# Optimization experiments

Measured on AMD Instinct MI355X. Metric: run time of the kernel, lower is better.

Reference implementation:

```python
import jax, jax.numpy as jnp
import numpy as np


def setup_inputs() -> dict:
    key = jax.random.key(0)
    k1, k2, k3, k4, k5 = jax.random.split(key, 5)
    N, L, H = 512, 512, 768
    num_texts = 32
    hidden_states = jax.random.normal(k1, (N, L, H), dtype=jnp.float32)
    attention_mask = jax.random.randint(k2, (N, L), 0, 2).astype(jnp.int32)
    sample_map = jnp.sort(jax.random.randint(k3, (N,), 0, num_texts).astype(jnp.int64))
    Wq = jax.random.normal(k4, (H, H), dtype=jnp.float32) * (1.0 / np.sqrt(H))
    bq = jnp.zeros((H,), dtype=jnp.float32)
    Wk = jax.random.normal(k5, (H, H), dtype=jnp.float32) * (1.0 / np.sqrt(H))
    bk = jnp.zeros((H,), dtype=jnp.float32)
    return {
        'hidden_states': hidden_states,
        'attention_mask': attention_mask,
        'sample_map': sample_map,
        'Wq': Wq, 'bq': bq, 'Wk': Wk, 'bk': bk,
        'num_texts': num_texts,
    }


def _attn_pool(hidden_states, mask, Wq, bq, Wk, bk):
    # hidden_states: [N, L, H]; mask: [N, L]
    H = hidden_states.shape[-1]
    # Q from mean over sequence (unmasked mean, as in original)
    q = jnp.einsum('nh,oh->no', hidden_states.mean(axis=1), Wq) + bq   # [N, H]
    k = jnp.einsum('nlh,oh->nlo', hidden_states, Wk) + bk              # [N, L, H]
    scores = jnp.einsum('nh,nlh->nl', q, k) / jnp.sqrt(jnp.float32(H))  # [N, L]
    scores = jnp.where(mask == 0, jnp.float32(-1e9), scores)
    alphas = jax.nn.softmax(scores, axis=1)                            # [N, L]
    return jnp.einsum('nl,nlh->nh', alphas, hidden_states)             # [N, H]


def reference(hidden_states, attention_mask, sample_map, Wq, bq, Wk, bk, num_texts):
    # dropout is identity in eval mode
    pooled = _attn_pool(hidden_states, attention_mask, Wq, bq, Wk, bk)  # [N, H]
    seg = sample_map.astype(jnp.int32)
    sums = jax.ops.segment_sum(pooled, seg, num_segments=num_texts)     # [T, H]
    counts = jax.ops.segment_sum(jnp.ones((pooled.shape[0],), pooled.dtype), seg,
                                 num_segments=num_texts)                # [T]
    counts = jnp.clip(counts, 1.0, None)
    return sums / counts[:, None]
```

## Files before the change

### kernel.cpp

```cpp
#include <hip/hip_runtime.h>
#include <math.h>

#define HDIM 768
#define LMAX 512

__device__ __forceinline__ float dot4(const float4 a, const float4 b) {
  return a.x * b.x + a.y * b.y + a.z * b.z + a.w * b.w;
}
__device__ __forceinline__ void fma4(float4& a, const float s, const float4 b) {
  a.x += s * b.x; a.y += s * b.y; a.z += s * b.z; a.w += s * b.w;
}
__device__ __forceinline__ void scale4(float4& a, const float s) {
  a.x *= s; a.y *= s; a.z *= s; a.w *= s;
}

__global__ void zero_flags(unsigned* flags) {
  if (threadIdx.x < 4) flags[threadIdx.x] = 0u;
}

__global__ __launch_bounds__(256) void detect_flags(const unsigned* __restrict__ mask_w,
                                                    const unsigned* __restrict__ smap_w,
                                                    unsigned* __restrict__ flags,
                                                    int mask_words, int smap_words) {
  const int gtid = blockIdx.x * blockDim.x + threadIdx.x;
  const int gsz = gridDim.x * blockDim.x;
  unsigned acc = 0;
  for (int i = gtid; i < mask_words / 2; i += gsz) acc |= mask_w[2 * i + 1];
  if (acc) atomicOr(&flags[0], 1u);
  unsigned acc2 = 0;
  for (int i = gtid; i < smap_words / 2; i += gsz) acc2 |= smap_w[2 * i + 1];
  if (acc2) atomicOr(&flags[1], 1u);
}

__global__ __launch_bounds__(384) void mean_kernel(const float* __restrict__ hs,
                                                   float* __restrict__ meanb, int L) {
  __shared__ float4 red2[HDIM / 4];
  const int n = blockIdx.x;
  const int tid = threadIdx.x;
  const int half = tid / 192, t = tid % 192;
  const float4* row = reinterpret_cast<const float4*>(hs) + (size_t)n * L * (HDIM / 4);
  float ax = 0.f, ay = 0.f, az = 0.f, aw = 0.f;
  int l = half;
  for (; l + 16 <= L; l += 16) {
    float4 u[8];
#pragma unroll
    for (int i = 0; i < 8; ++i) u[i] = row[(size_t)(l + 2 * i) * (HDIM / 4) + t];
#pragma unroll
    for (int i = 0; i < 8; ++i) { ax += u[i].x; ay += u[i].y; az += u[i].z; aw += u[i].w; }
  }
  for (; l < L; l += 2) {
    float4 u = row[(size_t)l * (HDIM / 4) + t];
    ax += u.x; ay += u.y; az += u.z; aw += u.w;
  }
  if (half == 1) { float4 o; o.x = ax; o.y = ay; o.z = az; o.w = aw; red2[t] = o; }
  __syncthreads();
  if (half == 0) {
    const float inv = 1.0f / (float)L;
    const float4 r = red2[t];
    float4 o;
    o.x = (ax + r.x) * inv; o.y = (ay + r.y) * inv;
    o.z = (az + r.z) * inv; o.w = (aw + r.w) * inv;
    reinterpret_cast<float4*>(meanb + (size_t)n * HDIM)[t] = o;
  }
}

__global__ __launch_bounds__(256) void gemm_bt(const float* __restrict__ A,
                                               const float* __restrict__ B,
                                               const float* __restrict__ bias,
                                               float* __restrict__ C,
                                               int M, int Nn, int K) {
  __shared__ float As[32][17];
  __shared__ float Bs[64][17];
  const int m0 = blockIdx.x * 32, n0 = blockIdx.y * 64;
  const int idx = threadIdx.x;
  const int lc = idx & 15, lr = idx >> 4;
  const int tc = idx & 15, tr = idx >> 4;
  float c[2][4] = {{0.f,0.f,0.f,0.f},{0.f,0.f,0.f,0.f}};
  for (int k0 = 0; k0 < K; k0 += 16) {
    __syncthreads();
    As[lr][lc]      = A[(size_t)(m0 + lr) * K + k0 + lc];
    As[lr + 16][lc] = A[(size_t)(m0 + lr + 16) * K + k0 + lc];
    Bs[lr][lc]      = B[(size_t)(n0 + lr) * K + k0 + lc];
    Bs[lr + 16][lc] = B[(size_t)(n0 + lr + 16) * K + k0 + lc];
    Bs[lr + 32][lc] = B[(size_t)(n0 + lr + 32) * K + k0 + lc];
    Bs[lr + 48][lc] = B[(size_t)(n0 + lr + 48) * K + k0 + lc];
    __syncthreads();
#pragma unroll
    for (int k = 0; k < 16; ++k) {
      const float a0 = As[tr * 2][k], a1 = As[tr * 2 + 1][k];
      const float b0 = Bs[tc * 4][k], b1 = Bs[tc * 4 + 1][k];
      const float b2 = Bs[tc * 4 + 2][k], b3 = Bs[tc * 4 + 3][k];
      c[0][0] += a0 * b0; c[0][1] += a0 * b1; c[0][2] += a0 * b2; c[0][3] += a0 * b3;
      c[1][0] += a1 * b0; c[1][1] += a1 * b1; c[1][2] += a1 * b2; c[1][3] += a1 * b3;
    }
  }
#pragma unroll
  for (int j = 0; j < 4; ++j) {
    const float bv = bias ? bias[n0 + tc * 4 + j] : 0.f;
    C[(size_t)(m0 + tr * 2) * Nn + n0 + tc * 4 + j]     = c[0][j] + bv;
    C[(size_t)(m0 + tr * 2 + 1) * Nn + n0 + tc * 4 + j] = c[1][j] + bv;
  }
}

__global__ __launch_bounds__(256) void gemm_bn(const float* __restrict__ A,
                                               const float* __restrict__ B,
                                               float* __restrict__ C,
                                               int M, int Nn, int K) {
  __shared__ float As[32][17];
  __shared__ float Bs[16][65];
  const int m0 = blockIdx.x * 32, n0 = blockIdx.y * 64;
  const int idx = threadIdx.x;
  const int lc = idx & 15, lr = idx >> 4;
  const int bc = idx & 63, br = idx >> 6;
  const int tc = idx & 15, tr = idx >> 4;
  float c[2][4] = {{0.f,0.f,0.f,0.f},{0.f,0.f,0.f,0.f}};
  for (int k0 = 0; k0 < K; k0 += 16) {
    __syncthreads();
    As[lr][lc]      = A[(size_t)(m0 + lr) * K + k0 + lc];
    As[lr + 16][lc] = A[(size_t)(m0 + lr + 16) * K + k0 + lc];
    Bs[br][bc]      = B[(size_t)(k0 + br) * Nn + n0 + bc];
    Bs[br + 4][bc]  = B[(size_t)(k0 + br + 4) * Nn + n0 + bc];
    Bs[br + 8][bc]  = B[(size_t)(k0 + br + 8) * Nn + n0 + bc];
    Bs[br + 12][bc] = B[(size_t)(k0 + br + 12) * Nn + n0 + bc];
    __syncthreads();
#pragma unroll
    for (int k = 0; k < 16; ++k) {
      const float a0 = As[tr * 2][k], a1 = As[tr * 2 + 1][k];
      const float b0 = Bs[k][tc * 4], b1 = Bs[k][tc * 4 + 1];
      const float b2 = Bs[k][tc * 4 + 2], b3 = Bs[k][tc * 4 + 3];
      c[0][0] += a0 * b0; c[0][1] += a0 * b1; c[0][2] += a0 * b2; c[0][3] += a0 * b3;
      c[1][0] += a1 * b0; c[1][1] += a1 * b1; c[1][2] += a1 * b2; c[1][3] += a1 * b3;
    }
  }
#pragma unroll
  for (int j = 0; j < 4; ++j) {
    C[(size_t)(m0 + tr * 2) * Nn + n0 + tc * 4 + j]     = c[0][j];
    C[(size_t)(m0 + tr * 2 + 1) * Nn + n0 + tc * 4 + j] = c[1][j];
  }
}

__global__ __launch_bounds__(256) void attnpool(const float* __restrict__ hs,
                                                const unsigned* __restrict__ mask_w,
                                                const float* __restrict__ v,
                                                const unsigned* __restrict__ flags,
                                                float* __restrict__ pooled, int L) {
  __shared__ int   mrow[LMAX];
  __shared__ float red[4][HDIM];
  __shared__ float mw[4], sw[4];
  const int n = gridDim.x - 1 - blockIdx.x;
  const int tid = threadIdx.x;
  const int w = tid >> 6, lane = tid & 63;

  const int mask_is_i32 = (flags[0] != 0);
  for (int t = tid; t < L; t += 256) {
    const size_t idx = (size_t)n * L + t;
    mrow[t] = (int)(mask_is_i32 ? mask_w[idx] : mask_w[2 * idx]);
  }

  const float4* v4 = reinterpret_cast<const float4*>(v + (size_t)n * HDIM);
  const float4 vf0 = v4[lane], vf1 = v4[64 + lane], vf2 = v4[128 + lane];
  const float4* hs4 = reinterpret_cast<const float4*>(hs) + (size_t)n * L * (HDIM / 4);
  const float scale = 1.0f / sqrtf((float)HDIM);

  const int rpw = L / 4;
  const int r0 = w * rpw;
  float4 A0 = {0,0,0,0}, A1 = {0,0,0,0}, A2 = {0,0,0,0};
  float m = -3.0e38f, ssum = 0.f;
  float4 xa[4][3], xb[4][3];

  auto loadg = [&](float4 (&X)[4][3], int g) {
    const float4* rp = hs4 + (size_t)(r0 + g * 4) * (HDIM / 4);
#pragma unroll
    for (int q = 0; q < 4; ++q) {
      X[q][0] = rp[q * (HDIM / 4) + lane];
      X[q][1] = rp[q * (HDIM / 4) + 64 + lane];
      X[q][2] = rp[q * (HDIM / 4) + 128 + lane];
    }
  };
  auto procg = [&](float4 (&X)[4][3], int g) {
    float s[4];
#pragma unroll
    for (int q = 0; q < 4; ++q) {
      float p = dot4(X[q][0], vf0) + dot4(X[q][1], vf1) + dot4(X[q][2], vf2);
#pragma unroll
      for (int off = 32; off > 0; off >>= 1) p += __shfl_xor(p, off, 64);
      s[q] = (mrow[r0 + g * 4 + q] == 0) ? -1e9f : p * scale;
    }
    const float mc = fmaxf(fmaxf(s[0], s[1]), fmaxf(s[2], s[3]));
    if (mc > m) {
      const float f = __expf(m - mc);
      ssum *= f; scale4(A0, f); scale4(A1, f); scale4(A2, f);
      m = mc;
    }
#pragma unroll
    for (int q = 0; q < 4; ++q) {
      const float pq = __expf(s[q] - m);
      ssum += pq;
      fma4(A0, pq, X[q][0]); fma4(A1, pq, X[q][1]); fma4(A2, pq, X[q][2]);
    }
  };

  __syncthreads();
  loadg(xa, 0);
  const int ng = rpw / 4;
  for (int g = 0; g < ng; g += 2) {
    loadg(xb, g + 1);
    procg(xa, g);
    if (g + 2 < ng) loadg(xa, g + 2);
    procg(xb, g + 1);
  }

  if (lane == 0) { mw[w] = m; sw[w] = ssum; }
  {
    float* rw = red[w];
    *reinterpret_cast<float4*>(rw + 4 * lane)       = A0;
    *reinterpret_cast<float4*>(rw + 256 + 4 * lane) = A1;
    *reinterpret_cast<float4*>(rw + 512 + 4 * lane) = A2;
  }
  __syncthreads();
  const float M = fmaxf(fmaxf(mw[0], mw[1]), fmaxf(mw[2], mw[3]));
  const float f0 = __expf(mw[0] - M), f1 = __expf(mw[1] - M);
  const float f2 = __expf(mw[2] - M), f3 = __expf(mw[3] - M);
  const float S = sw[0] * f0 + sw[1] * f1 + sw[2] * f2 + sw[3] * f3;
  const float inv = 1.0f / S;
#pragma unroll
  for (int part = 0; part < 3; ++part) {
    const int col = part * 256 + tid;
    const float o = red[0][col] * f0 + red[1][col] * f1 + red[2][col] * f2 + red[3][col] * f3;
    pooled[(size_t)n * HDIM + col] = o * inv;
  }
}

__global__ __launch_bounds__(256) void segmean(const float* __restrict__ pooled,
                                               const void* __restrict__ smap,
                                               const unsigned* __restrict__ flags,
                                               float* __restrict__ out, int N) {
  const int t = blockIdx.x, tid = threadIdx.x;
  const int col = blockIdx.y * 256 + tid;
  const int smap_is_i32 = (flags[1] != 0);
  float a = 0.f;
  int cnt = 0;
  for (int i = 0; i < N; ++i) {
    const int s = smap_is_i32 ? ((const int*)smap)[i]
                              : (int)((const long long*)smap)[i];
    if (s == t) { a += pooled[(size_t)i * HDIM + col]; ++cnt; }
  }
  out[(size_t)t * HDIM + col] = a / (float)(cnt > 0 ? cnt : 1);
}

extern "C" void kernel_launch(void* const* d_in, const int* in_sizes, int n_in,
                              void* d_out, int out_size, void* d_ws, size_t ws_size,
                              hipStream_t stream) {
  const float*    hs     = (const float*)d_in[0];
  const unsigned* mask_w = (const unsigned*)d_in[1];
  const void*     smap   = d_in[2];
  const float*    Wq     = (const float*)d_in[3];
  const float*    bq     = (const float*)d_in[4];
  const float*    Wk     = (const float*)d_in[5];

  const int N = in_sizes[2];
  const int L = in_sizes[1] / N;
  const int H = in_sizes[4];
  const int T = out_size / H;

  float* meanb  = (float*)d_ws;
  float* q      = meanb + (size_t)N * H;
  float* v      = q     + (size_t)N * H;
  float* pooled = v     + (size_t)N * H;
  unsigned* flags = (unsigned*)(pooled + (size_t)N * H);
  (void)ws_size; (void)n_in;

  zero_flags<<<1, 64, 0, stream>>>(flags);
  detect_flags<<<64, 256, 0, stream>>>(mask_w, (const unsigned*)smap, flags,
                                       N * L, N);
  mean_kernel<<<N, 384, 0, stream>>>(hs, meanb, L);
  gemm_bt<<<dim3(N / 32, H / 64), 256, 0, stream>>>(meanb, Wq, bq, q, N, H, H);
  gemm_bn<<<dim3(N / 32, H / 64), 256, 0, stream>>>(q, Wk, v, N, H, H);
  attnpool<<<N, 256, 0, stream>>>(hs, mask_w, v, flags, pooled, L);
  segmean<<<dim3(T, 3), 256, 0, stream>>>(pooled, smap, flags, (float*)d_out, N);
}
```

Measured before the change: 439.1 us.

## Split attention pooling across two blocks per sample with async LDS staging

The attention-pooling kernel now launches two blocks per sample, each covering half the sequence. Rows are staged into double-buffered shared memory with global_load_lds async copies, four rows per chunk, and each wave computes one row's score. Partial max, sum and accumulator are written per half and combined in a merged segment-mean kernel. Flag detection writes per-block slots instead of atomics, which drops the zero-flags launch. The new path adds two barriers per four-row chunk and a per-chunk shared-memory round trip, which may throttle a memory-bound streaming loop.

After: 442.5 us. About the same (+0.8%).

```diff
diff --git a/kernel.cpp b/kernel.cpp
--- a/kernel.cpp
+++ b/kernel.cpp
@@ -2,34 +2,35 @@
 #include <math.h>
 
 #define HDIM 768
-#define LMAX 512
+#define CH 4
 
 __device__ __forceinline__ float dot4(const float4 a, const float4 b) {
   return a.x * b.x + a.y * b.y + a.z * b.z + a.w * b.w;
 }
-__device__ __forceinline__ void fma4(float4& a, const float s, const float4 b) {
-  a.x += s * b.x; a.y += s * b.y; a.z += s * b.z; a.w += s * b.w;
-}
-__device__ __forceinline__ void scale4(float4& a, const float s) {
-  a.x *= s; a.y *= s; a.z *= s; a.w *= s;
-}
-
-__global__ void zero_flags(unsigned* flags) {
-  if (threadIdx.x < 4) flags[threadIdx.x] = 0u;
-}
-
-__global__ __launch_bounds__(256) void detect_flags(const unsigned* __restrict__ mask_w,
+
+__device__ __forceinline__ void async16(const float* g, float* l) {
+  __builtin_amdgcn_global_load_lds(
+      (const __attribute__((address_space(1))) void*)g,
+      (__attribute__((address_space(3))) void*)l, 16, 0, 0);
+}
+
+__global__ __launch_bounds__(256) void detect_slots(const unsigned* __restrict__ mask_w,
                                                     const unsigned* __restrict__ smap_w,
-                                                    unsigned* __restrict__ flags,
+                                                    unsigned* __restrict__ slots,
                                                     int mask_words, int smap_words) {
-  const int gtid = blockIdx.x * blockDim.x + threadIdx.x;
-  const int gsz = gridDim.x * blockDim.x;
+  __shared__ unsigned red[2];
+  const int b = blockIdx.x, tid = threadIdx.x;
+  if (tid < 2) red[tid] = 0;
+  __syncthreads();
+  const int gtid = b * 256 + tid, gsz = gridDim.x * 256;
   unsigned acc = 0;
   for (int i = gtid; i < mask_words / 2; i += gsz) acc |= mask_w[2 * i + 1];
-  if (acc) atomicOr(&flags[0], 1u);
   unsigned acc2 = 0;
   for (int i = gtid; i < smap_words / 2; i += gsz) acc2 |= smap_w[2 * i + 1];
-  if (acc2) atomicOr(&flags[1], 1u);
+  if (acc)  atomicOr(&red[0], 1u);
+  if (acc2) atomicOr(&red[1], 1u);
+  __syncthreads();
+  if (tid == 0) { slots[b] = red[0]; slots[64 + b] = red[1]; }
 }
 
 __global__ __launch_bounds__(384) void mean_kernel(const float* __restrict__ hs,
@@ -142,108 +143,121 @@
 __global__ __launch_bounds__(256) void attnpool(const float* __restrict__ hs,
                                                 const unsigned* __restrict__ mask_w,
                                                 const float* __restrict__ v,
-                                                const unsigned* __restrict__ flags,
-                                                float* __restrict__ pooled, int L) {
-  __shared__ int   mrow[LMAX];
-  __shared__ float red[4][HDIM];
-  __shared__ float mw[4], sw[4];
-  const int n = gridDim.x - 1 - blockIdx.x;
-  const int tid = threadIdx.x;
-  const int w = tid >> 6, lane = tid & 63;
-
-  const int mask_is_i32 = (flags[0] != 0);
-  for (int t = tid; t < L; t += 256) {
-    const size_t idx = (size_t)n * L + t;
+                                                const unsigned* __restrict__ slots,
+                                                float* __restrict__ acc_out,
+                                                float* __restrict__ ms_out, int L) {
+  __shared__ float buf[2][CH * HDIM];
+  __shared__ int   mrow[256];
+  __shared__ float sc[CH];
+  __shared__ unsigned mflag_sh;
+  const int bid = blockIdx.x;
+  const int n = (gridDim.x / 2 - 1) - (bid >> 1);
+  const int half = bid & 1;
+  const int tid = threadIdx.x, w = tid >> 6, lane = tid & 63;
+  const int Lh = L / 2, r0 = half * Lh;
+
+  if (tid == 0) {
+    unsigned f = 0;
+    for (int i = 0; i < 64; ++i) f |= slots[i];
+    mflag_sh = f;
+  }
+  __syncthreads();
+  const int mask_is_i32 = (mflag_sh != 0);
+  for (int t = tid; t < Lh; t += 256) {
+    const size_t idx = (size_t)n * L + r0 + t;
     mrow[t] = (int)(mask_is_i32 ? mask_w[idx] : mask_w[2 * idx]);
   }
 
   const float4* v4 = reinterpret_cast<const float4*>(v + (size_t)n * HDIM);
   const float4 vf0 = v4[lane], vf1 = v4[64 + lane], vf2 = v4[128 + lane];
-  const float4* hs4 = reinterpret_cast<const float4*>(hs) + (size_t)n * L * (HDIM / 4);
+  const float* base = hs + ((size_t)n * L + r0) * HDIM;
   const float scale = 1.0f / sqrtf((float)HDIM);
 
-  const int rpw = L / 4;
-  const int r0 = w * rpw;
-  float4 A0 = {0,0,0,0}, A1 = {0,0,0,0}, A2 = {0,0,0,0};
-  float m = -3.0e38f, ssum = 0.f;
-  float4 xa[4][3], xb[4][3];
-
-  auto loadg = [&](float4 (&X)[4][3], int g) {
-    const float4* rp = hs4 + (size_t)(r0 + g * 4) * (HDIM / 4);
-#pragma unroll
-    for (int q = 0; q < 4; ++q) {
-      X[q][0] = rp[q * (HDIM / 4) + lane];
-      X[q][1] = rp[q * (HDIM / 4) + 64 + lane];
-      X[q][2] = rp[q * (HDIM / 4) + 128 + lane];
+  auto stage = [&](int b, int c) {
+    const float* src = base + (size_t)c * (CH * HDIM);
+    float* dst = buf[b];
+#pragma unroll
+    for (int i = 0; i < 3; ++i) {
+      const int off = i * 1024 + w * 256;
+      async16(src + off + lane * 4, dst + off);
     }
   };
-  auto procg = [&](float4 (&X)[4][3], int g) {
-    float s[4];
-#pragma unroll
-    for (int q = 0; q < 4; ++q) {
-      float p = dot4(X[q][0], vf0) + dot4(X[q][1], vf1) + dot4(X[q][2], vf2);
+
+  stage(0, 0);
+  float m = -3.0e38f, ssum = 0.f, a0 = 0.f, a1 = 0.f, a2 = 0.f;
+  const int nch = Lh / CH;
+
+  for (int c = 0; c < nch; ++c) {
+    asm volatile("s_waitcnt vmcnt(0) lgkmcnt(0)" ::: "memory");
+    __builtin_amdgcn_s_barrier();
+    if (c + 1 < nch) stage((c + 1) & 1, c + 1);
+    const float* cb = buf[c & 1];
+
+    {
+      const float4* rp = reinterpret_cast<const float4*>(cb + w * HDIM);
+      float p = dot4(rp[lane], vf0) + dot4(rp[64 + lane], vf1) + dot4(rp[128 + lane], vf2);
 #pragma unroll
       for (int off = 32; off > 0; off >>= 1) p += __shfl_xor(p, off, 64);
-      s[q] = (mrow[r0 + g * 4 + q] == 0) ? -1e9f : p * scale;
-    }
-    const float mc = fmaxf(fmaxf(s[0], s[1]), fmaxf(s[2], s[3]));
+      float s = (mrow[c * CH + w] == 0) ? -1e9f : p * scale;
+      if (lane == 0) sc[w] = s;
+    }
+    asm volatile("s_waitcnt lgkmcnt(0)" ::: "memory");
+    __builtin_amdgcn_s_barrier();
+
+    const float s0 = sc[0], s1 = sc[1], s2 = sc[2], s3 = sc[3];
+    const float mc = fmaxf(fmaxf(s0, s1), fmaxf(s2, s3));
     if (mc > m) {
       const float f = __expf(m - mc);
-      ssum *= f; scale4(A0, f); scale4(A1, f); scale4(A2, f);
+      ssum *= f; a0 *= f; a1 *= f; a2 *= f;
       m = mc;
     }
-#pragma unroll
-    for (int q = 0; q < 4; ++q) {
-      const float pq = __expf(s[q] - m);
-      ssum += pq;
-      fma4(A0, pq, X[q][0]); fma4(A1, pq, X[q][1]); fma4(A2, pq, X[q][2]);
-    }
-  };
-
-  __syncthreads();
-  loadg(xa, 0);
-  const int ng = rpw / 4;
-  for (int g = 0; g < ng; g += 2) {
-    loadg(xb, g + 1);
-    procg(xa, g);
-    if (g + 2 < ng) loadg(xa, g + 2);
-    procg(xb, g + 1);
-  }
-
-  if (lane == 0) { mw[w] = m; sw[w] = ssum; }
-  {
-    float* rw = red[w];
-    *reinterpret_cast<float4*>(rw + 4 * lane)       = A0;
-    *reinterpret_cast<float4*>(rw + 256 + 4 * lane) = A1;
-    *reinterpret_cast<float4*>(rw + 512 + 4 * lane) = A2;
-  }
-  __syncthreads();
-  const float M = fmaxf(fmaxf(mw[0], mw[1]), fmaxf(mw[2], mw[3]));
-  const float f0 = __expf(mw[0] - M), f1 = __expf(mw[1] - M);
-  const float f2 = __expf(mw[2] - M), f3 = __expf(mw[3] - M);
-  const float S = sw[0] * f0 + sw[1] * f1 + sw[2] * f2 + sw[3] * f3;
-  const float inv = 1.0f / S;
-#pragma unroll
-  for (int part = 0; part < 3; ++part) {
-    const int col = part * 256 + tid;
-    const float o = red[0][col] * f0 + red[1][col] * f1 + red[2][col] * f2 + red[3][col] * f3;
-    pooled[(size_t)n * HDIM + col] = o * inv;
-  }
-}
-
-__global__ __launch_bounds__(256) void segmean(const float* __restrict__ pooled,
-                                               const void* __restrict__ smap,
-                                               const unsigned* __restrict__ flags,
-                                               float* __restrict__ out, int N) {
+    const float p0 = __expf(s0 - m), p1 = __expf(s1 - m);
+    const float p2 = __expf(s2 - m), p3 = __expf(s3 - m);
+    ssum += p0 + p1 + p2 + p3;
+    a0 += p0 * cb[tid]             + p1 * cb[HDIM + tid]
+        + p2 * cb[2 * HDIM + tid]  + p3 * cb[3 * HDIM + tid];
+    a1 += p0 * cb[256 + tid]            + p1 * cb[HDIM + 256 + tid]
+        + p2 * cb[2 * HDIM + 256 + tid] + p3 * cb[3 * HDIM + 256 + tid];
+    a2 += p0 * cb[512 + tid]            + p1 * cb[HDIM + 512 + tid]
+        + p2 * cb[2 * HDIM + 512 + tid] + p3 * cb[3 * HDIM + 512 + tid];
+  }
+
+  const int pidx = n * 2 + half;
+  acc_out[(size_t)pidx * HDIM + tid]       = a0;
+  acc_out[(size_t)pidx * HDIM + 256 + tid] = a1;
+  acc_out[(size_t)pidx * HDIM + 512 + tid] = a2;
+  if (tid == 0) { ms_out[pidx * 2] = m; ms_out[pidx * 2 + 1] = ssum; }
+}
+
+__global__ __launch_bounds__(256) void merge_segmean(const float* __restrict__ acc,
+                                                     const float* __restrict__ ms,
+                                                     const void* __restrict__ smap,
+                                                     const unsigned* __restrict__ slots_s,
+                                                     float* __restrict__ out, int N) {
+  __shared__ unsigned fsh;
   const int t = blockIdx.x, tid = threadIdx.x;
   const int col = blockIdx.y * 256 + tid;
-  const int smap_is_i32 = (flags[1] != 0);
+  if (tid == 0) {
+    unsigned f = 0;
+    for (int i = 0; i < 64; ++i) f |= slots_s[i];
+    fsh = f;
+  }
+  __syncthreads();
+  const int smap_is_i32 = (fsh != 0);
   float a = 0.f;
   int cnt = 0;
   for (int i = 0; i < N; ++i) {
     const int s = smap_is_i32 ? ((const int*)smap)[i]
                               : (int)((const long long*)smap)[i];
-    if (s == t) { a += pooled[(size_t)i * HDIM + col]; ++cnt; }
+    if (s != t) continue;
+    const float m0 = ms[(i * 2) * 2],     q0 = ms[(i * 2) * 2 + 1];
+    const float m1 = ms[(i * 2 + 1) * 2], q1 = ms[(i * 2 + 1) * 2 + 1];
+    const float M = fmaxf(m0, m1);
+    const float f0 = __expf(m0 - M), f1 = __expf(m1 - M);
+    const float S = q0 * f0 + q1 * f1;
+    const float o = (acc[(size_t)(i * 2) * HDIM + col] * f0 +
+                     acc[(size_t)(i * 2 + 1) * HDIM + col] * f1) / S;
+    a += o; ++cnt;
   }
   out[(size_t)t * HDIM + col] = a / (float)(cnt > 0 ? cnt : 1);
 }
@@ -262,20 +276,20 @@
   const int L = in_sizes[1] / N;
   const int H = in_sizes[4];
   const int T = out_size / H;
-
-  float* meanb  = (float*)d_ws;
-  float* q      = meanb + (size_t)N * H;
-  float* v      = q     + (size_t)N * H;
-  float* pooled = v     + (size_t)N * H;
-  unsigned* flags = (unsigned*)(pooled + (size_t)N * H);
+  const size_t NH = (size_t)N * H;
+
+  float* meanb = (float*)d_ws;
+  float* q     = meanb + NH;
+  float* v     = q + NH;
+  float* acc   = v + NH;
+  float* ms    = acc + 2 * NH;
+  unsigned* slots = (unsigned*)(ms + 4 * N);
   (void)ws_size; (void)n_in;
 
-  zero_flags<<<1, 64, 0, stream>>>(flags);
-  detect_flags<<<64, 256, 0, stream>>>(mask_w, (const unsigned*)smap, flags,
-                                       N * L, N);
+  detect_slots<<<64, 256, 0, stream>>>(mask_w, (const unsigned*)smap, slots, N * L, N);
   mean_kernel<<<N, 384, 0, stream>>>(hs, meanb, L);
   gemm_bt<<<dim3(N / 32, H / 64), 256, 0, stream>>>(meanb, Wq, bq, q, N, H, H);
   gemm_bn<<<dim3(N / 32, H / 64), 256, 0, stream>>>(q, Wk, v, N, H, H);
-  attnpool<<<N, 256, 0, stream>>>(hs, mask_w, v, flags, pooled, L);
-  segmean<<<dim3(T, 3), 256, 0, stream>>>(pooled, smap, flags, (float*)d_out, N);
-}
+  attnpool<<<2 * N, 256, 0, stream>>>(hs, mask_w, v, slots, acc, ms, L);
+  merge_segmean<<<dim3(T, 3), 256, 0, stream>>>(acc, ms, smap, slots + 64, (float*)d_out, N);
+}
```

## Fold Wq and Wk into one weight and fuse mean, projection and attention pooling

Applied to the files above, without the earlier changes.

Uses the identity q·k = mean·(Wqᵀ Wk)·h + bqᵀ Wk·h. A weight-only kernel precomputes Wc = Wqᵀ Wk and the bias vector c0, which removes the two per-sample GEMMs. A single per-sample kernel then computes the sequence mean, does the Wc matvec in-block and runs the online-softmax pooling. The pooling pass walks the rows in reverse so the second read of hidden_states can hit recently cached data. The flag detection no longer needs a zeroing kernel because each block writes its own slot. The trade-offs are that every block re-reads the 768×768 Wc from cache, and the pooling loop count of 88 is hard-coded, which assumes L is at most about 528.

Result: faster. 419.7 us (-4.4%).

```diff
diff --git a/kernel.cpp b/kernel.cpp
--- a/kernel.cpp
+++ b/kernel.cpp
@@ -2,6 +2,7 @@
 #include <math.h>
 
 #define HDIM 768
+#define NG   192
 #define LMAX 512
 
 __device__ __forceinline__ float dot4(const float4 a, const float4 b) {
@@ -14,230 +15,230 @@
   a.x *= s; a.y *= s; a.z *= s; a.w *= s;
 }
 
-__global__ void zero_flags(unsigned* flags) {
-  if (threadIdx.x < 4) flags[threadIdx.x] = 0u;
-}
-
-__global__ __launch_bounds__(256) void detect_flags(const unsigned* __restrict__ mask_w,
+__global__ __launch_bounds__(256) void detect_slots(const unsigned* __restrict__ mask_w,
                                                     const unsigned* __restrict__ smap_w,
-                                                    unsigned* __restrict__ flags,
+                                                    unsigned* __restrict__ slots,
                                                     int mask_words, int smap_words) {
-  const int gtid = blockIdx.x * blockDim.x + threadIdx.x;
-  const int gsz = gridDim.x * blockDim.x;
+  __shared__ unsigned red[2];
+  const int b = blockIdx.x, tid = threadIdx.x;
+  if (tid < 2) red[tid] = 0;
+  __syncthreads();
+  const int gtid = b * 256 + tid, gsz = gridDim.x * 256;
   unsigned acc = 0;
   for (int i = gtid; i < mask_words / 2; i += gsz) acc |= mask_w[2 * i + 1];
-  if (acc) atomicOr(&flags[0], 1u);
   unsigned acc2 = 0;
   for (int i = gtid; i < smap_words / 2; i += gsz) acc2 |= smap_w[2 * i + 1];
-  if (acc2) atomicOr(&flags[1], 1u);
-}
-
-__global__ __launch_bounds__(384) void mean_kernel(const float* __restrict__ hs,
-                                                   float* __restrict__ meanb, int L) {
-  __shared__ float4 red2[HDIM / 4];
-  const int n = blockIdx.x;
-  const int tid = threadIdx.x;
-  const int half = tid / 192, t = tid % 192;
-  const float4* row = reinterpret_cast<const float4*>(hs) + (size_t)n * L * (HDIM / 4);
+  if (acc)  atomicOr(&red[0], 1u);
+  if (acc2) atomicOr(&red[1], 1u);
+  __syncthreads();
+  if (tid == 0) { slots[b] = red[0]; slots[64 + b] = red[1]; }
+}
+
+__global__ __launch_bounds__(256) void prep_wc(const float* __restrict__ Wq,
+                                               const float* __restrict__ Wk,
+                                               const float* __restrict__ bq,
+                                               float* __restrict__ Wc,
+                                               float* __restrict__ c0, int H) {
+  __shared__ float As[16][33];
+  __shared__ float Bs[16][65];
+  __shared__ float bqs[16];
+  const int i0 = blockIdx.x * 32, j0 = blockIdx.y * 64;
+  const int idx = threadIdx.x;
+  const int li = idx & 31, lk = idx >> 5;
+  const int lj = idx & 63, lk2 = idx >> 6;
+  const int tc = idx & 15, tr = idx >> 4;
+  float c[2][4] = {{0.f,0.f,0.f,0.f},{0.f,0.f,0.f,0.f}};
+  float cb[4] = {0.f,0.f,0.f,0.f};
+  const bool bias_lane = (blockIdx.x == 0) && (tr == 0);
+  for (int o0 = 0; o0 < H; o0 += 16) {
+    __syncthreads();
+    As[lk][li]       = Wq[(size_t)(o0 + lk) * H + i0 + li];
+    As[lk + 8][li]   = Wq[(size_t)(o0 + lk + 8) * H + i0 + li];
+    Bs[lk2][lj]      = Wk[(size_t)(o0 + lk2) * H + j0 + lj];
+    Bs[lk2 + 4][lj]  = Wk[(size_t)(o0 + lk2 + 4) * H + j0 + lj];
+    Bs[lk2 + 8][lj]  = Wk[(size_t)(o0 + lk2 + 8) * H + j0 + lj];
+    Bs[lk2 + 12][lj] = Wk[(size_t)(o0 + lk2 + 12) * H + j0 + lj];
+    if (idx < 16) bqs[idx] = bq[o0 + idx];
+    __syncthreads();
+#pragma unroll
+    for (int k = 0; k < 16; ++k) {
+      const float a0 = As[k][tr * 2], a1 = As[k][tr * 2 + 1];
+      const float b0 = Bs[k][tc * 4],     b1 = Bs[k][tc * 4 + 1];
+      const float b2 = Bs[k][tc * 4 + 2], b3 = Bs[k][tc * 4 + 3];
+      c[0][0] += a0 * b0; c[0][1] += a0 * b1; c[0][2] += a0 * b2; c[0][3] += a0 * b3;
+      c[1][0] += a1 * b0; c[1][1] += a1 * b1; c[1][2] += a1 * b2; c[1][3] += a1 * b3;
+      if (bias_lane) {
+        const float bv = bqs[k];
+        cb[0] += bv * b0; cb[1] += bv * b1; cb[2] += bv * b2; cb[3] += bv * b3;
+      }
+    }
+  }
+#pragma unroll
+  for (int j = 0; j < 4; ++j) {
+    Wc[(size_t)(i0 + tr * 2) * H + j0 + tc * 4 + j]     = c[0][j];
+    Wc[(size_t)(i0 + tr * 2 + 1) * H + j0 + tc * 4 + j] = c[1][j];
+  }
+  if (bias_lane) {
+#pragma unroll
+    for (int j = 0; j < 4; ++j) c0[j0 + tc * 4 + j] = cb[j];
+  }
+}
+
+__global__ __launch_bounds__(384) void fused(const float* __restrict__ hs,
+                                             const unsigned* __restrict__ mask_w,
+                                             const float* __restrict__ Wc,
+                                             const float* __restrict__ c0,
+                                             const unsigned* __restrict__ slots,
+                                             float* __restrict__ pooled, int L) {
+  __shared__ float4 red2[NG];
+  __shared__ float4 meanv4[NG];
+  __shared__ float4 vv4[NG];
+  __shared__ float4 redv4[6][NG];
+  __shared__ float mw[6], sw[6];
+  __shared__ int   mrow[LMAX];
+  __shared__ unsigned mfl;
+  const int n = blockIdx.x, tid = threadIdx.x;
+  const int w = tid >> 6, lane = tid & 63;
+
+  if (tid == 0) mfl = 0u;
+  __syncthreads();
+  if (tid < 64 && slots[tid]) atomicOr(&mfl, 1u);
+
+  const int half = tid / NG, t = tid - half * NG;
+  const float4* hb = reinterpret_cast<const float4*>(hs) + (size_t)n * L * NG;
   float ax = 0.f, ay = 0.f, az = 0.f, aw = 0.f;
   int l = half;
   for (; l + 16 <= L; l += 16) {
     float4 u[8];
 #pragma unroll
-    for (int i = 0; i < 8; ++i) u[i] = row[(size_t)(l + 2 * i) * (HDIM / 4) + t];
+    for (int i = 0; i < 8; ++i) u[i] = hb[(size_t)(l + 2 * i) * NG + t];
 #pragma unroll
     for (int i = 0; i < 8; ++i) { ax += u[i].x; ay += u[i].y; az += u[i].z; aw += u[i].w; }
   }
   for (; l < L; l += 2) {
-    float4 u = row[(size_t)l * (HDIM / 4) + t];
+    float4 u = hb[(size_t)l * NG + t];
     ax += u.x; ay += u.y; az += u.z; aw += u.w;
   }
   if (half == 1) { float4 o; o.x = ax; o.y = ay; o.z = az; o.w = aw; red2[t] = o; }
   __syncthreads();
+
   if (half == 0) {
     const float inv = 1.0f / (float)L;
     const float4 r = red2[t];
     float4 o;
     o.x = (ax + r.x) * inv; o.y = (ay + r.y) * inv;
     o.z = (az + r.z) * inv; o.w = (aw + r.w) * inv;
-    reinterpret_cast<float4*>(meanb + (size_t)n * HDIM)[t] = o;
-  }
-}
-
-__global__ __launch_bounds__(256) void gemm_bt(const float* __restrict__ A,
-                                               const float* __restrict__ B,
-                                               const float* __restrict__ bias,
-                                               float* __restrict__ C,
-                                               int M, int Nn, int K) {
-  __shared__ float As[32][17];
-  __shared__ float Bs[64][17];
-  const int m0 = blockIdx.x * 32, n0 = blockIdx.y * 64;
-  const int idx = threadIdx.x;
-  const int lc = idx & 15, lr = idx >> 4;
-  const int tc = idx & 15, tr = idx >> 4;
-  float c[2][4] = {{0.f,0.f,0.f,0.f},{0.f,0.f,0.f,0.f}};
-  for (int k0 = 0; k0 < K; k0 += 16) {
-    __syncthreads();
-    As[lr][lc]      = A[(size_t)(m0 + lr) * K + k0 + lc];
-    As[lr + 16][lc] = A[(size_t)(m0 + lr + 16) * K + k0 + lc];
-    Bs[lr][lc]      = B[(size_t)(n0 + lr) * K + k0 + lc];
-    Bs[lr + 16][lc] = B[(size_t)(n0 + lr + 16) * K + k0 + lc];
-    Bs[lr + 32][lc] = B[(size_t)(n0 + lr + 32) * K + k0 + lc];
-    Bs[lr + 48][lc] = B[(size_t)(n0 + lr + 48) * K + k0 + lc];
-    __syncthreads();
-#pragma unroll
-    for (int k = 0; k < 16; ++k) {
-      const float a0 = As[tr * 2][k], a1 = As[tr * 2 + 1][k];
-      const float b0 = Bs[tc * 4][k], b1 = Bs[tc * 4 + 1][k];
-      const float b2 = Bs[tc * 4 + 2][k], b3 = Bs[tc * 4 + 3][k];
-      c[0][0] += a0 * b0; c[0][1] += a0 * b1; c[0][2] += a0 * b2; c[0][3] += a0 * b3;
-      c[1][0] += a1 * b0; c[1][1] += a1 * b1; c[1][2] += a1 * b2; c[1][3] += a1 * b3;
-    }
-  }
-#pragma unroll
-  for (int j = 0; j < 4; ++j) {
-    const float bv = bias ? bias[n0 + tc * 4 + j] : 0.f;
-    C[(size_t)(m0 + tr * 2) * Nn + n0 + tc * 4 + j]     = c[0][j] + bv;
-    C[(size_t)(m0 + tr * 2 + 1) * Nn + n0 + tc * 4 + j] = c[1][j] + bv;
-  }
-}
-
-__global__ __launch_bounds__(256) void gemm_bn(const float* __restrict__ A,
-                                               const float* __restrict__ B,
-                                               float* __restrict__ C,
-                                               int M, int Nn, int K) {
-  __shared__ float As[32][17];
-  __shared__ float Bs[16][65];
-  const int m0 = blockIdx.x * 32, n0 = blockIdx.y * 64;
-  const int idx = threadIdx.x;
-  const int lc = idx & 15, lr = idx >> 4;
-  const int bc = idx & 63, br = idx >> 6;
-  const int tc = idx & 15, tr = idx >> 4;
-  float c[2][4] = {{0.f,0.f,0.f,0.f},{0.f,0.f,0.f,0.f}};
-  for (int k0 = 0; k0 < K; k0 += 16) {
-    __syncthreads();
-    As[lr][lc]      = A[(size_t)(m0 + lr) * K + k0 + lc];
-    As[lr + 16][lc] = A[(size_t)(m0 + lr + 16) * K + k0 + lc];
-    Bs[br][bc]      = B[(size_t)(k0 + br) * Nn + n0 + bc];
-    Bs[br + 4][bc]  = B[(size_t)(k0 + br + 4) * Nn + n0 + bc];
-    Bs[br + 8][bc]  = B[(size_t)(k0 + br + 8) * Nn + n0 + bc];
-    Bs[br + 12][bc] = B[(size_t)(k0 + br + 12) * Nn + n0 + bc];
-    __syncthreads();
-#pragma unroll
-    for (int k = 0; k < 16; ++k) {
-      const float a0 = As[tr * 2][k], a1 = As[tr * 2 + 1][k];
-      const float b0 = Bs[k][tc * 4], b1 = Bs[k][tc * 4 + 1];
-      const float b2 = Bs[k][tc * 4 + 2], b3 = Bs[k][tc * 4 + 3];
-      c[0][0] += a0 * b0; c[0][1] += a0 * b1; c[0][2] += a0 * b2; c[0][3] += a0 * b3;
-      c[1][0] += a1 * b0; c[1][1] += a1 * b1; c[1][2] += a1 * b2; c[1][3] += a1 * b3;
-    }
-  }
-#pragma unroll
-  for (int j = 0; j < 4; ++j) {
-    C[(size_t)(m0 + tr * 2) * Nn + n0 + tc * 4 + j]     = c[0][j];
-    C[(size_t)(m0 + tr * 2 + 1) * Nn + n0 + tc * 4 + j] = c[1][j];
-  }
-}
-
-__global__ __launch_bounds__(256) void attnpool(const float* __restrict__ hs,
-                                                const unsigned* __restrict__ mask_w,
-                                                const float* __restrict__ v,
-                                                const unsigned* __restrict__ flags,
-                                                float* __restrict__ pooled, int L) {
-  __shared__ int   mrow[LMAX];
-  __shared__ float red[4][HDIM];
-  __shared__ float mw[4], sw[4];
-  const int n = gridDim.x - 1 - blockIdx.x;
-  const int tid = threadIdx.x;
-  const int w = tid >> 6, lane = tid & 63;
-
-  const int mask_is_i32 = (flags[0] != 0);
-  for (int t = tid; t < L; t += 256) {
-    const size_t idx = (size_t)n * L + t;
-    mrow[t] = (int)(mask_is_i32 ? mask_w[idx] : mask_w[2 * idx]);
-  }
-
-  const float4* v4 = reinterpret_cast<const float4*>(v + (size_t)n * HDIM);
-  const float4 vf0 = v4[lane], vf1 = v4[64 + lane], vf2 = v4[128 + lane];
-  const float4* hs4 = reinterpret_cast<const float4*>(hs) + (size_t)n * L * (HDIM / 4);
+    meanv4[t] = o;
+  }
+  const int mask_is_i32 = (mfl != 0);
+  for (int tt = tid; tt < L; tt += 384) {
+    const size_t idx = (size_t)n * L + tt;
+    mrow[tt] = (int)(mask_is_i32 ? mask_w[idx] : mask_w[2 * idx]);
+  }
+  __syncthreads();
+
+  {
+    const int c1 = tid, c2 = tid + 384;
+    float acc1 = 0.f, acc2 = 0.f;
+    const float* wp = Wc;
+    for (int o = 0; o < HDIM; o += 4) {
+      const float4 mv = meanv4[o >> 2];
+      acc1 += mv.x * wp[c1] + mv.y * wp[HDIM + c1] + mv.z * wp[2 * HDIM + c1] + mv.w * wp[3 * HDIM + c1];
+      acc2 += mv.x * wp[c2] + mv.y * wp[HDIM + c2] + mv.z * wp[2 * HDIM + c2] + mv.w * wp[3 * HDIM + c2];
+      wp += 4 * HDIM;
+    }
+    ((float*)vv4)[c1] = acc1 + c0[c1];
+    ((float*)vv4)[c2] = acc2 + c0[c2];
+  }
+  __syncthreads();
+
+  const float4 vf0 = vv4[lane], vf1 = vv4[64 + lane], vf2 = vv4[128 + lane];
   const float scale = 1.0f / sqrtf((float)HDIM);
-
-  const int rpw = L / 4;
-  const int r0 = w * rpw;
+  const int cnt = (L - 1 - w) / 6 + 1;
+  float m = -3.0e38f, ss = 0.f;
   float4 A0 = {0,0,0,0}, A1 = {0,0,0,0}, A2 = {0,0,0,0};
-  float m = -3.0e38f, ssum = 0.f;
-  float4 xa[4][3], xb[4][3];
-
-  auto loadg = [&](float4 (&X)[4][3], int g) {
-    const float4* rp = hs4 + (size_t)(r0 + g * 4) * (HDIM / 4);
-#pragma unroll
-    for (int q = 0; q < 4; ++q) {
-      X[q][0] = rp[q * (HDIM / 4) + lane];
-      X[q][1] = rp[q * (HDIM / 4) + 64 + lane];
-      X[q][2] = rp[q * (HDIM / 4) + 128 + lane];
+  float4 xa[2][3], xb[2][3];
+
+  auto ld = [&](float4 (&X)[2][3], int j) {
+#pragma unroll
+    for (int u = 0; u < 2; ++u) {
+      const int jj = j + u;
+      const int rr = (jj < cnt) ? (L - 1 - 6 * jj - w) : 0;
+      const float4* rp = hb + (size_t)rr * NG;
+      X[u][0] = rp[lane]; X[u][1] = rp[64 + lane]; X[u][2] = rp[128 + lane];
     }
   };
-  auto procg = [&](float4 (&X)[4][3], int g) {
-    float s[4];
-#pragma unroll
-    for (int q = 0; q < 4; ++q) {
-      float p = dot4(X[q][0], vf0) + dot4(X[q][1], vf1) + dot4(X[q][2], vf2);
+  auto pr = [&](float4 (&X)[2][3], int j) {
+    float s[2]; bool val[2];
+#pragma unroll
+    for (int u = 0; u < 2; ++u) {
+      const int jj = j + u;
+      val[u] = (jj < cnt);
+      const int r = L - 1 - 6 * jj - w;
+      float p = dot4(X[u][0], vf0) + dot4(X[u][1], vf1) + dot4(X[u][2], vf2);
 #pragma unroll
       for (int off = 32; off > 0; off >>= 1) p += __shfl_xor(p, off, 64);
-      s[q] = (mrow[r0 + g * 4 + q] == 0) ? -1e9f : p * scale;
-    }
-    const float mc = fmaxf(fmaxf(s[0], s[1]), fmaxf(s[2], s[3]));
+      s[u] = (!val[u] || mrow[r & (LMAX - 1)] == 0) ? -1e9f : p * scale;
+    }
+    const float mc = fmaxf(s[0], s[1]);
     if (mc > m) {
       const float f = __expf(m - mc);
-      ssum *= f; scale4(A0, f); scale4(A1, f); scale4(A2, f);
+      ss *= f; scale4(A0, f); scale4(A1, f); scale4(A2, f);
       m = mc;
     }
 #pragma unroll
-    for (int q = 0; q < 4; ++q) {
-      const float pq = __expf(s[q] - m);
-      ssum += pq;
-      fma4(A0, pq, X[q][0]); fma4(A1, pq, X[q][1]); fma4(A2, pq, X[q][2]);
+    for (int u = 0; u < 2; ++u) {
+      const float pq = val[u] ? __expf(s[u] - m) : 0.f;
+      ss += pq;
+      fma4(A0, pq, X[u][0]); fma4(A1, pq, X[u][1]); fma4(A2, pq, X[u][2]);
     }
   };
 
-  __syncthreads();
-  loadg(xa, 0);
-  const int ng = rpw / 4;
-  for (int g = 0; g < ng; g += 2) {
-    loadg(xb, g + 1);
-    procg(xa, g);
-    if (g + 2 < ng) loadg(xa, g + 2);
-    procg(xb, g + 1);
-  }
-
-  if (lane == 0) { mw[w] = m; sw[w] = ssum; }
-  {
-    float* rw = red[w];
-    *reinterpret_cast<float4*>(rw + 4 * lane)       = A0;
-    *reinterpret_cast<float4*>(rw + 256 + 4 * lane) = A1;
-    *reinterpret_cast<float4*>(rw + 512 + 4 * lane) = A2;
-  }
-  __syncthreads();
-  const float M = fmaxf(fmaxf(mw[0], mw[1]), fmaxf(mw[2], mw[3]));
-  const float f0 = __expf(mw[0] - M), f1 = __expf(mw[1] - M);
-  const float f2 = __expf(mw[2] - M), f3 = __expf(mw[3] - M);
-  const float S = sw[0] * f0 + sw[1] * f1 + sw[2] * f2 + sw[3] * f3;
-  const float inv = 1.0f / S;
-#pragma unroll
-  for (int part = 0; part < 3; ++part) {
-    const int col = part * 256 + tid;
-    const float o = red[0][col] * f0 + red[1][col] * f1 + red[2][col] * f2 + red[3][col] * f3;
-    pooled[(size_t)n * HDIM + col] = o * inv;
+  ld(xa, 0);
+  for (int j = 0; j < 88; j += 4) {
+    ld(xb, j + 2);
+    pr(xa, j);
+    if (j + 4 < 88) ld(xa, j + 4);
+    pr(xb, j + 2);
+  }
+
+  if (lane == 0) { mw[w] = m; sw[w] = ss; }
+  redv4[w][lane]       = A0;
+  redv4[w][64 + lane]  = A1;
+  redv4[w][128 + lane] = A2;
+  __syncthreads();
+  float M = mw[0];
+#pragma unroll
+  for (int j = 1; j < 6; ++j) M = fmaxf(M, mw[j]);
+  float f[6], S = 0.f;
+#pragma unroll
+  for (int j = 0; j < 6; ++j) { f[j] = __expf(mw[j] - M); S += sw[j] * f[j]; }
+  const float invS = 1.0f / S;
+  const float* redp = (const float*)redv4;
+#pragma unroll
+  for (int part = 0; part < 2; ++part) {
+    const int col = part * 384 + tid;
+    float o = 0.f;
+#pragma unroll
+    for (int j = 0; j < 6; ++j) o += redp[j * HDIM + col] * f[j];
+    pooled[(size_t)n * HDIM + col] = o * invS;
   }
 }
 
 __global__ __launch_bounds__(256) void segmean(const float* __restrict__ pooled,
                                                const void* __restrict__ smap,
-                                               const unsigned* __restrict__ flags,
+                                               const unsigned* __restrict__ slots_s,
                                                float* __restrict__ out, int N) {
+  __shared__ unsigned fsh;
   const int t = blockIdx.x, tid = threadIdx.x;
   const int col = blockIdx.y * 256 + tid;
-  const int smap_is_i32 = (flags[1] != 0);
+  if (tid == 0) {
+    unsigned f = 0;
+    for (int i = 0; i < 64; ++i) f |= slots_s[i];
+    fsh = f;
+  }
+  __syncthreads();
+  const int smap_is_i32 = (fsh != 0);
   float a = 0.f;
   int cnt = 0;
   for (int i = 0; i < N; ++i) {
@@ -263,19 +264,14 @@
   const int H = in_sizes[4];
   const int T = out_size / H;
 
-  float* meanb  = (float*)d_ws;
-  float* q      = meanb + (size_t)N * H;
-  float* v      = q     + (size_t)N * H;
-  float* pooled = v     + (size_t)N * H;
-  unsigned* flags = (unsigned*)(pooled + (size_t)N * H);
+  float* Wc     = (float*)d_ws;
+  float* c0     = Wc + (size_t)H * H;
+  float* pooled = c0 + H;
+  unsigned* slots = (unsigned*)(pooled + (size_t)N * H);
   (void)ws_size; (void)n_in;
 
-  zero_flags<<<1, 64, 0, stream>>>(flags);
-  detect_flags<<<64, 256, 0, stream>>>(mask_w, (const unsigned*)smap, flags,
-                                       N * L, N);
-  mean_kernel<<<N, 384, 0, stream>>>(hs, meanb, L);
-  gemm_bt<<<dim3(N / 32, H / 64), 256, 0, stream>>>(meanb, Wq, bq, q, N, H, H);
-  gemm_bn<<<dim3(N / 32, H / 64), 256, 0, stream>>>(q, Wk, v, N, H, H);
-  attnpool<<<N, 256, 0, stream>>>(hs, mask_w, v, flags, pooled, L);
-  segmean<<<dim3(T, 3), 256, 0, stream>>>(pooled, smap, flags, (float*)d_out, N);
-}
+  detect_slots<<<64, 256, 0, stream>>>(mask_w, (const unsigned*)smap, slots, N * L, N);
+  prep_wc<<<dim3(H / 32, H / 64), 256, 0, stream>>>(Wq, Wk, bq, Wc, c0, H);
+  fused<<<N, 384, 0, stream>>>(hs, mask_w, Wc, c0, slots, pooled, L);
+  segmean<<<dim3(T, 3), 256, 0, stream>>>(pooled, smap, slots + 64, (float*)d_out, N);
+}
```
